# Kernel optimization log

Hardware: AMD Instinct MI355X
Metric: run time of the kernel (lower is better)

The kernel has to match this reference:

```python
import jax, jax.numpy as jnp
import numpy as np

B, N, C, T, K = 32, 4096, 768, 1000, 20

def setup_inputs() -> dict:
    key = jax.random.key(0)
    k1, k2, k3, k4 = jax.random.split(key, 4)
    g_feat = jax.random.normal(k1, (B, 1, C), dtype=jnp.float32)
    inp = jax.random.normal(k2, (B, N, C), dtype=jnp.float32)
    tau = jax.random.uniform(k3, (1,), dtype=jnp.float32)
    text_embeddings = jax.random.normal(k4, (T, C), dtype=jnp.float32) * 0.01
    return {"g_feat": g_feat, "input": inp, "tau": tau, "text_embeddings": text_embeddings}


def reference(g_feat, input, tau, text_embeddings):
    feat = input  # [B, N, C]
    # 1x1 conv of global feature against text embeddings -> class logits [B, T]
    vg_logit = jnp.einsum('bc,tc->bt', g_feat[:, 0, :], text_embeddings)
    # top-20 candidate categories per image
    _, indices = jax.lax.top_k(vg_logit, K)              # [B, K]
    agg_text_features = text_embeddings[indices]          # [B, K, C] gather
    # per-pixel logits against the 20 gathered text embeddings
    seg_logit = jnp.exp(tau[0]) * jnp.einsum('bkc,bnc->bkn', agg_text_features, feat)  # [B, K, N]
    # hard (straight-through) softmax over candidate axis (dim=-2)
    y_soft = jax.nn.softmax(seg_logit, axis=-2)
    idx = jnp.argmax(seg_logit, axis=-2)                  # [B, N]
    y_hard = jnp.moveaxis(jax.nn.one_hot(idx, K, dtype=seg_logit.dtype), -1, -2)  # [B, K, N]
    attn = y_hard - jax.lax.stop_gradient(y_soft) + y_soft
    # normalize over pixel axis (assign_eps = 1.0)
    assign_attn = attn / (jnp.sum(attn, axis=-1, keepdims=True) + 1.0)
    # combine: [B, N, K] @ [B, K, C] -> [B, N, C]
    text_grids = jnp.einsum('bkn,bkc->bnc', assign_attn, agg_text_features)
    return text_grids
```

## Files before the change

kernel.cpp:

```cpp
#include <hip/hip_runtime.h>
#include <cfloat>

#define B_ 32
#define N_ 4096
#define C_ 768
#define T_ 1000
#define K_ 20

#define PXB 256
#define PHC 32
#define NPH (C_/PHC)
#define GAP_TH 1e-4f
#define MAXF 16384

typedef float f32x4 __attribute__((ext_vector_type(4)));
typedef int   i32x2 __attribute__((ext_vector_type(2)));
typedef short s16x8 __attribute__((ext_vector_type(8)));

__device__ __forceinline__ unsigned short bf_rne(float x) {
    unsigned u = __float_as_uint(x);
    return (unsigned short)((u + 0x7fffu + ((u >> 16) & 1u)) >> 16);
}

__global__ __launch_bounds__(256) void k1_logits(const float* __restrict__ g_feat,
                                                 const float* __restrict__ text,
                                                 double* __restrict__ logits,
                                                 int* __restrict__ cnt,
                                                 int* __restrict__ flagcnt) {
    int b = blockIdx.x;
    int wid = threadIdx.x >> 6, lane = threadIdx.x & 63;
    int t = blockIdx.y * 4 + wid;
    if (b == 0 && blockIdx.y == 0) {
        for (int i = threadIdx.x; i < B_ * K_; i += 256) cnt[i] = 0;
        if (threadIdx.x == 0) flagcnt[0] = 0;
    }
    const float* g = g_feat + b * C_;
    const float* e = text + t * C_;
    double s = 0.0;
    #pragma unroll
    for (int j = 0; j < 12; ++j) {
        int c = lane + 64 * j;
        s += (double)g[c] * (double)e[c];
    }
    #pragma unroll
    for (int m = 32; m; m >>= 1) s += __shfl_xor(s, m);
    if (lane == 0) logits[b * T_ + t] = s;
}

__global__ __launch_bounds__(256) void k1b_topk(const double* __restrict__ logits,
                                                const float* __restrict__ text,
                                                float* __restrict__ agg,
                                                unsigned short* __restrict__ Epk) {
    __shared__ unsigned short hiL[32 * C_];
    __shared__ unsigned short loL[32 * C_];
    __shared__ int ssel[K_];
    int b = blockIdx.x, tid = threadIdx.x, lane = tid & 63;
    if (tid < 64) {
        double v[16];
        #pragma unroll
        for (int j = 0; j < 16; ++j) {
            int t = lane + 64 * j;
            v[j] = (t < T_) ? logits[b * T_ + t] : -DBL_MAX;
        }
        for (int it = 0; it < K_; ++it) {
            double bv = -DBL_MAX; int bi = 0x7fffffff;
            #pragma unroll
            for (int j = 0; j < 16; ++j) {
                int t = lane + 64 * j;
                if (v[j] > bv) { bv = v[j]; bi = t; }
            }
            #pragma unroll
            for (int m = 32; m; m >>= 1) {
                double ov = __shfl_xor(bv, m); int oi = __shfl_xor(bi, m);
                if (ov > bv || (ov == bv && oi < bi)) { bv = ov; bi = oi; }
            }
            if (lane == 0) ssel[it] = bi;
            #pragma unroll
            for (int j = 0; j < 16; ++j) {
                int t = lane + 64 * j;
                if (t == bi) v[j] = -DBL_MAX;
            }
        }
    }
    __syncthreads();
    for (int i = tid; i < 32 * C_; i += 256) {
        int r = i / C_, c = i - r * C_;
        float v = (r < K_) ? text[ssel[r] * C_ + c] : 0.f;
        if (r < K_) agg[b * K_ * C_ + i] = v;
        unsigned u = __float_as_uint(v);
        float fh = __uint_as_float(u & 0xffff0000u);
        hiL[i] = (unsigned short)(u >> 16);
        loL[i] = bf_rne(v - fh);
    }
    __syncthreads();
    for (int i = tid; i < 24 * 256; i += 256) {
        int p = i >> 8, r = i & 255, f = r >> 6, ln = r & 63;
        int row = (f & 1) * 16 + (ln & 15);
        int col = p * 32 + (ln >> 4) * 8;
        const unsigned short* src = ((f < 2) ? hiL : loL) + row * C_ + col;
        *(s16x8*)(Epk + ((size_t)b * 6144 + i) * 8) = *(const s16x8*)src;
    }
}

__global__ __launch_bounds__(256, 2) void k2_argmax(const float* __restrict__ feat,
                                                    const unsigned short* __restrict__ Epk,
                                                    int* __restrict__ kidx,
                                                    int* __restrict__ cnt,
                                                    int* __restrict__ flagcnt,
                                                    int* __restrict__ flaglist) {
    __shared__ unsigned short hiT[2][PXB * PHC];
    __shared__ unsigned short loT[2][PXB * PHC];
    __shared__ int scnt[K_];
    int bx = blockIdx.x;
    int b = bx >> 4, tile = bx & 15;
    int n0 = tile * PXB;
    int tid = threadIdx.x, wid = tid >> 6, lane = tid & 63;
    if (tid < K_) scnt[tid] = 0;
    __syncthreads();

    const float* fb = feat + ((size_t)b * N_ + n0) * C_;
    const unsigned short* Eb = Epk + (size_t)b * 6144 * 8;
    int l3 = lane >> 3;
    int ch = lane & 7;
    int arow = lane & 15, acg = lane >> 4;

    f32x4 fr[8];
    auto LOADF = [&](int p) {
        #pragma unroll
        for (int i = 0; i < 8; ++i) {
            int row = wid * 64 + i * 8 + l3;
            fr[i] = *(const f32x4*)(fb + (size_t)row * C_ + p * PHC + ch * 4);
        }
    };
    auto CVTW = [&](int buf) {
        int g = ch >> 1, h = ch & 1;
        #pragma unroll
        for (int i = 0; i < 8; ++i) {
            int row = wid * 64 + i * 8 + l3;
            unsigned u0 = __float_as_uint(fr[i].x), u1 = __float_as_uint(fr[i].y);
            unsigned u2 = __float_as_uint(fr[i].z), u3 = __float_as_uint(fr[i].w);
            unsigned ha = (u0 >> 16) | (u1 & 0xffff0000u);
            unsigned hb = (u2 >> 16) | (u3 & 0xffff0000u);
            unsigned la = (unsigned)bf_rne(fr[i].x - __uint_as_float(u0 & 0xffff0000u)) |
                          ((unsigned)bf_rne(fr[i].y - __uint_as_float(u1 & 0xffff0000u)) << 16);
            unsigned lb = (unsigned)bf_rne(fr[i].z - __uint_as_float(u2 & 0xffff0000u)) |
                          ((unsigned)bf_rne(fr[i].w - __uint_as_float(u3 & 0xffff0000u)) << 16);
            int a16 = row * PHC + ((g ^ (row & 3)) * 8) + h * 4;
            i32x2 hv = { (int)ha, (int)hb };
            i32x2 lv = { (int)la, (int)lb };
            *(i32x2*)&hiT[buf][a16] = hv;
            *(i32x2*)&loT[buf][a16] = lv;
        }
    };

    s16x8 Ach0, Ach1, Acl0, Acl1, Anh0, Anh1, Anl0, Anl1;
    auto LOADA = [&](int p, s16x8& h0, s16x8& h1, s16x8& l0, s16x8& l1) {
        const s16x8* ap = (const s16x8*)(Eb + (size_t)p * 256 * 8);
        h0 = ap[0 * 64 + lane];
        h1 = ap[1 * 64 + lane];
        l0 = ap[2 * 64 + lane];
        l1 = ap[3 * 64 + lane];
    };

    f32x4 acc0[4], acc1[4];
    #pragma unroll
    for (int i = 0; i < 4; ++i) { acc0[i] = (f32x4)0.f; acc1[i] = (f32x4)0.f; }

    LOADF(0);
    CVTW(0);
    LOADF(1);
    LOADA(0, Ach0, Ach1, Acl0, Acl1);
    LOADA(1, Anh0, Anh1, Anl0, Anl1);

    #pragma unroll 1
    for (int p = 0; p < NPH; ++p) {
        int cur = p & 1;
        if (p + 1 < NPH) {
            CVTW(cur ^ 1);
            if (p + 2 < NPH) LOADF(p + 2);
        }
        asm volatile("s_waitcnt lgkmcnt(0)" ::: "memory");
        __builtin_amdgcn_sched_barrier(0);

        #pragma unroll
        for (int i = 0; i < 4; ++i) {
            int px = wid * 64 + i * 16 + arow;
            int a16 = px * PHC + (acg ^ (px & 3)) * 8;
            s16x8 Bh = *(const s16x8*)&hiT[cur][a16];
            s16x8 Bl = *(const s16x8*)&loT[cur][a16];
            acc0[i] = __builtin_amdgcn_mfma_f32_16x16x32_bf16(Ach0, Bh, acc0[i], 0, 0, 0);
            acc1[i] = __builtin_amdgcn_mfma_f32_16x16x32_bf16(Ach1, Bh, acc1[i], 0, 0, 0);
            acc0[i] = __builtin_amdgcn_mfma_f32_16x16x32_bf16(Ach0, Bl, acc0[i], 0, 0, 0);
            acc1[i] = __builtin_amdgcn_mfma_f32_16x16x32_bf16(Ach1, Bl, acc1[i], 0, 0, 0);
            acc0[i] = __builtin_amdgcn_mfma_f32_16x16x32_bf16(Acl0, Bh, acc0[i], 0, 0, 0);
            acc1[i] = __builtin_amdgcn_mfma_f32_16x16x32_bf16(Acl1, Bh, acc1[i], 0, 0, 0);
        }

        Ach0 = Anh0; Ach1 = Anh1; Acl0 = Anl0; Acl1 = Anl1;
        if (p + 2 < NPH) LOADA(p + 2, Anh0, Anh1, Anl0, Anl1);
    }

    #pragma unroll
    for (int i = 0; i < 4; ++i) {
        int kb = acg * 4;
        float m1 = acc0[i][0]; int i1 = kb; float m2 = -FLT_MAX;
        #pragma unroll
        for (int r = 1; r < 4; ++r) {
            float v = acc0[i][r];
            if (v > m1) { m2 = m1; m1 = v; i1 = kb + r; }
            else if (v > m2) m2 = v;
        }
        if (acg == 0) {
            #pragma unroll
            for (int r = 0; r < 4; ++r) {
                float v = acc1[i][r];
                if (v > m1) { m2 = m1; m1 = v; i1 = 16 + r; }
                else if (v > m2) m2 = v;
            }
        }
        #pragma unroll
        for (int s = 16; s < 64; s <<= 1) {
            float om1 = __shfl_xor(m1, s); int oi1 = __shfl_xor(i1, s);
            float om2 = __shfl_xor(m2, s);
            if (om1 > m1 || (om1 == m1 && oi1 < i1)) { m2 = fmaxf(m1, om2); m1 = om1; i1 = oi1; }
            else { m2 = fmaxf(m2, om1); }
        }
        if (lane < 16) {
            int n = n0 + wid * 64 + i * 16 + lane;
            kidx[b * N_ + n] = i1;
            atomicAdd(&scnt[i1], 1);
            if (m1 - m2 < GAP_TH) {
                int pos = atomicAdd(flagcnt, 1);
                if (pos < MAXF) flaglist[pos] = b * N_ + n;
            }
        }
    }
    __syncthreads();
    if (tid < K_) atomicAdd(&cnt[b * K_ + tid], scnt[tid]);
}

__global__ __launch_bounds__(256) void k25_refine(const float* __restrict__ feat,
                                                  const float* __restrict__ agg,
                                                  int* __restrict__ kidx,
                                                  int* __restrict__ cnt,
                                                  const int* __restrict__ flagcnt,
                                                  const int* __restrict__ flaglist) {
    int wid = threadIdx.x >> 6, lane = threadIdx.x & 63;
    int wg = blockIdx.x * 4 + wid;
    int nf = flagcnt[0]; if (nf > MAXF) nf = MAXF;
    for (int e = wg; e < nf; e += gridDim.x * 4) {
        int pix = flaglist[e];
        int b = pix >> 12;
        const float* fr = feat + (size_t)pix * C_;
        const float* ebase = agg + b * K_ * C_;
        double fd[12];
        #pragma unroll
        for (int j = 0; j < 12; ++j) fd[j] = (double)fr[lane + 64 * j];
        double best = -DBL_MAX; int bi = 0;
        for (int k = 0; k < K_; ++k) {
            const float* er = ebase + k * C_;
            double s = 0.0;
            #pragma unroll
            for (int j = 0; j < 12; ++j) s += fd[j] * (double)er[lane + 64 * j];
            #pragma unroll
            for (int m = 32; m; m >>= 1) s += __shfl_xor(s, m);
            if (s > best) { best = s; bi = k; }
        }
        if (lane == 0) {
            int old = kidx[pix];
            if (old != bi) {
                kidx[pix] = bi;
                atomicSub(&cnt[b * K_ + old], 1);
                atomicAdd(&cnt[b * K_ + bi], 1);
            }
        }
    }
}

__global__ __launch_bounds__(256) void k3s_scale(const float* __restrict__ agg,
                                                 const int* __restrict__ cnt,
                                                 float* __restrict__ sagg) {
    __shared__ float sc[K_];
    int b = blockIdx.x, tid = threadIdx.x;
    if (tid < K_) sc[tid] = 1.0f / ((float)cnt[b * K_ + tid] + 1.0f);
    __syncthreads();
    const f32x4* a4 = (const f32x4*)(agg + (size_t)b * K_ * C_);
    f32x4* s4 = (f32x4*)(sagg + (size_t)b * K_ * C_);
    #pragma unroll 1
    for (int i = tid; i < K_ * (C_ / 4); i += 256) {
        int k = i / (C_ / 4);
        s4[i] = a4[i] * sc[k];
    }
}

__global__ __launch_bounds__(256) void k4_out(const float* __restrict__ sagg,
                                              const int* __restrict__ kidx,
                                              float* __restrict__ out) {
    int wid = threadIdx.x >> 6, lane = threadIdx.x & 63;
    int wg = blockIdx.x * 4 + wid;
    int base = wg * 8;
    int b = base >> 12;
    int kk[8];
    #pragma unroll
    for (int i = 0; i < 8; ++i) kk[i] = kidx[base + i];
    const f32x4* sagg4 = (const f32x4*)sagg;
    f32x4* out4 = (f32x4*)out;

    f32x4 va0, va1, va2, vb0, vb1, vb2;
    {
        const f32x4* a4 = sagg4 + (size_t)(b * K_ + kk[0]) * (C_ / 4);
        va0 = a4[lane]; va1 = a4[lane + 64]; va2 = a4[lane + 128];
    }
    #pragma unroll
    for (int i = 0; i < 8; ++i) {
        if (i + 1 < 8) {
            const f32x4* a4 = sagg4 + (size_t)(b * K_ + kk[i + 1]) * (C_ / 4);
            vb0 = a4[lane]; vb1 = a4[lane + 64]; vb2 = a4[lane + 128];
        }
        f32x4* o4 = out4 + (size_t)(base + i) * (C_ / 4);
        o4[lane] = va0; o4[lane + 64] = va1; o4[lane + 128] = va2;
        va0 = vb0; va1 = vb1; va2 = vb2;
    }
}

extern "C" void kernel_launch(void* const* d_in, const int* in_sizes, int n_in,
                              void* d_out, int out_size, void* d_ws, size_t ws_size,
                              hipStream_t stream) {
    const float* g_feat = (const float*)d_in[0];
    const float* feat   = (const float*)d_in[1];
    const float* text   = (const float*)d_in[3];
    float* out = (float*)d_out;

    char* ws = (char*)d_ws;
    double* logits        = (double*)(ws + 0);
    float*  agg           = (float*) (ws + 262144);
    int*    cnt           = (int*)   (ws + 2230784);
    int*    flagc         = (int*)   (ws + 2233344);
    int*    flagl         = (int*)   (ws + 2233408);
    int*    kidx          = (int*)   (ws + 2301504);
    unsigned short* Epk   = (unsigned short*)(ws + 2825792);
    float*  sagg          = (float*) (ws + 5971520);

    k1_logits<<<dim3(32, 250), 256, 0, stream>>>(g_feat, text, logits, cnt, flagc);
    k1b_topk<<<32, 256, 0, stream>>>(logits, text, agg, Epk);
    k2_argmax<<<32 * 16, 256, 0, stream>>>(feat, Epk, kidx, cnt, flagc, flagl);
    k25_refine<<<1024, 256, 0, stream>>>(feat, agg, kidx, cnt, flagc, flagl);
    k3s_scale<<<32, 256, 0, stream>>>(agg, cnt, sagg);
    k4_out<<<4096, 256, 0, stream>>>(sagg, kidx, out);
}
```

Measured before the change: 273.0 us.

## Single-buffer LDS tiles and drop A prefetch to run four blocks per CU

In the argmax GEMM kernel, the double-buffered hi/lo LDS tiles become single buffers, which halves LDS use. The next-phase A-fragment prefetch registers are removed and A is loaded at the start of each phase. Launch bounds go from 2 to 4 blocks per CU so more waves can hide memory latency. In exchange, feature loads are now prefetched only one phase ahead instead of two, and the A-load latency is exposed inside each phase.

```diff
diff --git a/kernel.cpp b/kernel.cpp
--- a/kernel.cpp
+++ b/kernel.cpp
@@ -102,14 +102,14 @@
     }
 }
 
-__global__ __launch_bounds__(256, 2) void k2_argmax(const float* __restrict__ feat,
+__global__ __launch_bounds__(256, 4) void k2_argmax(const float* __restrict__ feat,
                                                     const unsigned short* __restrict__ Epk,
                                                     int* __restrict__ kidx,
                                                     int* __restrict__ cnt,
                                                     int* __restrict__ flagcnt,
                                                     int* __restrict__ flaglist) {
-    __shared__ unsigned short hiT[2][PXB * PHC];
-    __shared__ unsigned short loT[2][PXB * PHC];
+    __shared__ unsigned short hiT[PXB * PHC];
+    __shared__ unsigned short loT[PXB * PHC];
     __shared__ int scnt[K_];
     int bx = blockIdx.x;
     int b = bx >> 4, tile = bx & 15;
@@ -132,7 +132,7 @@
             fr[i] = *(const f32x4*)(fb + (size_t)row * C_ + p * PHC + ch * 4);
         }
     };
-    auto CVTW = [&](int buf) {
+    auto CVTW = [&]() {
         int g = ch >> 1, h = ch & 1;
         #pragma unroll
         for (int i = 0; i < 8; ++i) {
@@ -148,18 +148,18 @@
             int a16 = row * PHC + ((g ^ (row & 3)) * 8) + h * 4;
             i32x2 hv = { (int)ha, (int)hb };
             i32x2 lv = { (int)la, (int)lb };
-            *(i32x2*)&hiT[buf][a16] = hv;
-            *(i32x2*)&loT[buf][a16] = lv;
+            *(i32x2*)&hiT[a16] = hv;
+            *(i32x2*)&loT[a16] = lv;
         }
     };
 
-    s16x8 Ach0, Ach1, Acl0, Acl1, Anh0, Anh1, Anl0, Anl1;
-    auto LOADA = [&](int p, s16x8& h0, s16x8& h1, s16x8& l0, s16x8& l1) {
+    s16x8 Ach0, Ach1, Acl0, Acl1;
+    auto LOADA = [&](int p) {
         const s16x8* ap = (const s16x8*)(Eb + (size_t)p * 256 * 8);
-        h0 = ap[0 * 64 + lane];
-        h1 = ap[1 * 64 + lane];
-        l0 = ap[2 * 64 + lane];
-        l1 = ap[3 * 64 + lane];
+        Ach0 = ap[0 * 64 + lane];
+        Ach1 = ap[1 * 64 + lane];
+        Acl0 = ap[2 * 64 + lane];
+        Acl1 = ap[3 * 64 + lane];
     };
 
     f32x4 acc0[4], acc1[4];
@@ -167,18 +167,14 @@
     for (int i = 0; i < 4; ++i) { acc0[i] = (f32x4)0.f; acc1[i] = (f32x4)0.f; }
 
     LOADF(0);
-    CVTW(0);
-    LOADF(1);
-    LOADA(0, Ach0, Ach1, Acl0, Acl1);
-    LOADA(1, Anh0, Anh1, Anl0, Anl1);
 
     #pragma unroll 1
     for (int p = 0; p < NPH; ++p) {
-        int cur = p & 1;
-        if (p + 1 < NPH) {
-            CVTW(cur ^ 1);
-            if (p + 2 < NPH) LOADF(p + 2);
-        }
+        LOADA(p);
+        asm volatile("s_waitcnt lgkmcnt(0)" ::: "memory");
+        __builtin_amdgcn_sched_barrier(0);
+        CVTW();
+        if (p + 1 < NPH) LOADF(p + 1);
         asm volatile("s_waitcnt lgkmcnt(0)" ::: "memory");
         __builtin_amdgcn_sched_barrier(0);
 
@@ -186,8 +182,8 @@
         for (int i = 0; i < 4; ++i) {
             int px = wid * 64 + i * 16 + arow;
             int a16 = px * PHC + (acg ^ (px & 3)) * 8;
-            s16x8 Bh = *(const s16x8*)&hiT[cur][a16];
-            s16x8 Bl = *(const s16x8*)&loT[cur][a16];
+            s16x8 Bh = *(const s16x8*)&hiT[a16];
+            s16x8 Bl = *(const s16x8*)&loT[a16];
             acc0[i] = __builtin_amdgcn_mfma_f32_16x16x32_bf16(Ach0, Bh, acc0[i], 0, 0, 0);
             acc1[i] = __builtin_amdgcn_mfma_f32_16x16x32_bf16(Ach1, Bh, acc1[i], 0, 0, 0);
             acc0[i] = __builtin_amdgcn_mfma_f32_16x16x32_bf16(Ach0, Bl, acc0[i], 0, 0, 0);
@@ -195,9 +191,6 @@
             acc0[i] = __builtin_amdgcn_mfma_f32_16x16x32_bf16(Acl0, Bh, acc0[i], 0, 0, 0);
             acc1[i] = __builtin_amdgcn_mfma_f32_16x16x32_bf16(Acl1, Bh, acc1[i], 0, 0, 0);
         }
-
-        Ach0 = Anh0; Ach1 = Anh1; Acl0 = Anl0; Acl1 = Anl1;
-        if (p + 2 < NPH) LOADA(p + 2, Anh0, Anh1, Anl0, Anl1);
     }
 
     #pragma unroll
```

Result: no change. 272.3 us (-0.2%).
